# Performance work log

Hardware: AMD Instinct MI355X
Metric: run time of the kernel (lower is better)

The kernel has to match this reference:

```python
import jax, jax.numpy as jnp
import numpy as np

B, T, C, U, W = 8, 2048, 512, 512, 2


def setup_inputs() -> dict:
    key = jax.random.key(0)
    k1, k2 = jax.random.split(key)
    x = jax.random.normal(k1, (B, T, C), dtype=jnp.float32)
    # Conv1D kernel: [window, in_channels, 3*units] (z, f, o gates), glorot-ish scale
    kernel = jax.random.normal(k2, (W, C, 3 * U), dtype=jnp.float32) * (1.0 / np.sqrt(W * C))
    bias = jnp.zeros((3 * U,), dtype=jnp.float32)
    initial_state = jnp.zeros((1, U), dtype=jnp.float32)
    return {"x": x, "kernel": kernel, "bias": bias, "initial_state": initial_state}


def reference(x, kernel, bias, initial_state):
    # Causal Conv1D: pad (window-1) on the left of the time axis.
    window = kernel.shape[0]
    gates = jax.lax.conv_general_dilated(
        x, kernel,
        window_strides=(1,),
        padding=[(window - 1, 0)],
        dimension_numbers=("NWC", "WIO", "NWC"),
    ) + bias  # [B, T, 3U]
    z, f, o = jnp.split(gates, 3, axis=-1)
    z = jnp.tanh(z)
    f = jax.nn.sigmoid(f)
    o = jax.nn.sigmoid(o)

    # fo-pool recurrence: h_t = f_t * h_{t-1} + (1 - f_t) * z_t
    h0 = jnp.repeat(initial_state, x.shape[0], axis=0)  # [B, U]
    fs = jnp.moveaxis(f, 1, 0)  # [T, B, U]
    zs = jnp.moveaxis(z, 1, 0)  # [T, B, U]

    def step(h, fz):
        f_t, z_t = fz
        h = f_t * h + (1.0 - f_t) * z_t
        return h, h

    _, hs = jax.lax.scan(step, h0, (fs, zs))  # hs: [T, B, U]
    recurrent = jnp.moveaxis(hs, 0, 1)  # [B, T, U]

    # output gate, return_sequences=True
    return recurrent * o
```

## Files before the change

kernel.cpp:

```cpp
#include <hip/hip_runtime.h>


#define Bn 8
#define Tn 2048
#define Cn 512
#define Un 512
#define Nn 1536
#define Kn 1024
#define Mn (Bn * Tn)
#define NC 32
#define CL 64

using bf16x8 = __attribute__((ext_vector_type(8))) __bf16;
using f32x4  = __attribute__((ext_vector_type(4))) float;
using us8    = __attribute__((ext_vector_type(8))) unsigned short;

__device__ __forceinline__ void async16(const void* g, void* l) {
  __builtin_amdgcn_global_load_lds((const __attribute__((address_space(1))) void*)g,
                                   (__attribute__((address_space(3))) void*)l, 16, 0, 0);
}

__device__ __forceinline__ unsigned short f2bf(float v) {
  union { float f; unsigned u; } c; c.f = v;
  unsigned u = c.u;
  return (unsigned short)((u + 0x7fffu + ((u >> 16) & 1u)) >> 16);
}
__device__ __forceinline__ float asf(unsigned u) {
  union { unsigned u; float f; } c; c.u = u; return c.f;
}
__device__ __forceinline__ float bf_lo(unsigned w) { return asf(w << 16); }
__device__ __forceinline__ float bf_hi(unsigned w) { return asf(w & 0xffff0000u); }

__device__ __forceinline__ float fast_sigmoid(float x) {
  float e = __builtin_amdgcn_exp2f(-1.4426950408889634f * x);
  return __builtin_amdgcn_rcpf(1.0f + e);
}
__device__ __forceinline__ float fast_tanh(float x) {
  float e = __builtin_amdgcn_exp2f(-2.8853900817779268f * x);
  return 2.0f * __builtin_amdgcn_rcpf(1.0f + e) - 1.0f;
}

__global__ __launch_bounds__(256) void conv_x(const float* __restrict__ x,
                                              unsigned short* __restrict__ xb) {
  int idx = blockIdx.x * 256 + threadIdx.x;
  int c8  = idx & 63;
  int row = idx >> 6;
  int b   = row / (Tn + 1);
  int t   = row - b * (Tn + 1);
  us8 ov;
  if (t == 0) {
    ov = (us8)0;
  } else {
    const float* src = x + (size_t)(b * Tn + t - 1) * Cn + c8 * 8;
    float4 v0 = *(const float4*)src;
    float4 v1 = *(const float4*)(src + 4);
    ov[0] = f2bf(v0.x); ov[1] = f2bf(v0.y); ov[2] = f2bf(v0.z); ov[3] = f2bf(v0.w);
    ov[4] = f2bf(v1.x); ov[5] = f2bf(v1.y); ov[6] = f2bf(v1.z); ov[7] = f2bf(v1.w);
  }
  *(us8*)(xb + (size_t)row * Cn + c8 * 8) = ov;
}

__global__ __launch_bounds__(256) void conv_k(const float* __restrict__ kern,
                                              unsigned short* __restrict__ kT) {
  __shared__ float tile[32][33];
  int kb = blockIdx.x, nb = blockIdx.y;
  int tx = threadIdx.x & 31, ty = threadIdx.x >> 5;
#pragma unroll
  for (int i = 0; i < 4; i++)
    tile[ty + i * 8][tx] = kern[(size_t)(kb * 32 + ty + i * 8) * Nn + nb * 32 + tx];
  __syncthreads();
#pragma unroll
  for (int i = 0; i < 4; i++) {
    int n = nb * 32 + ty + i * 8;
    int k = kb * 32 + tx;
    kT[(size_t)n * Kn + k] = f2bf(tile[tx][ty + i * 8]);
  }
}

__global__ __launch_bounds__(256) void gemm_gates(const unsigned short* __restrict__ xb,
                                                  const unsigned short* __restrict__ kT,
                                                  const float* __restrict__ bias,
                                                  unsigned short* __restrict__ gates) {
  __shared__ unsigned short As[128 * 64];
  __shared__ unsigned short Bs[128 * 64];
  const int tid = threadIdx.x;
  const int m0 = blockIdx.x * 128;
  const int n0 = blockIdx.y * 128;
  const int batch = m0 / Tn;
  const int lane = tid & 63;
  const int w = tid >> 6, wr = w >> 1, wc = w & 1;

  const int srow = (w << 3) + (lane >> 3);
  const int skq  = (lane & 7) ^ (lane >> 3);
  const unsigned short* aStage = xb + (size_t)(m0 + batch + srow) * Cn + (skq << 3);
  const unsigned short* bStage = kT + (size_t)(n0 + srow) * Kn + (skq << 3);

  f32x4 zero = {0.f, 0.f, 0.f, 0.f};
  f32x4 acc[4][4];
#pragma unroll
  for (int i = 0; i < 4; i++)
#pragma unroll
    for (int j = 0; j < 4; j++) acc[i][j] = zero;

  const int rA0 = wr * 64 + (lane & 15);
  const int rB0 = wc * 64 + (lane & 15);
  const int swz = lane & 7;

  for (int k0 = 0; k0 < Kn; k0 += 64) {
#pragma unroll
    for (int j = 0; j < 4; j++) {
      async16(aStage + (size_t)(j << 5) * Cn + k0, &As[(j * 256 + tid) * 8]);
      async16(bStage + (size_t)(j << 5) * Kn + k0, &Bs[(j * 256 + tid) * 8]);
    }
    __builtin_amdgcn_s_waitcnt(0);
    __syncthreads();

#pragma unroll
    for (int ks = 0; ks < 2; ks++) {
      const int col = (((ks << 2) + (lane >> 4)) ^ swz) << 3;
      bf16x8 af[4], bf[4];
#pragma unroll
      for (int i = 0; i < 4; i++) {
        af[i] = *(const bf16x8*)&As[(rA0 + i * 16) * 64 + col];
        bf[i] = *(const bf16x8*)&Bs[(rB0 + i * 16) * 64 + col];
      }
#pragma unroll
      for (int i = 0; i < 4; i++)
#pragma unroll
        for (int j = 0; j < 4; j++)
          acc[i][j] = __builtin_amdgcn_mfma_f32_16x16x32_bf16(af[i], bf[j], acc[i][j], 0, 0, 0);
    }
    __syncthreads();
  }

  const int region = blockIdx.y >> 2;
  const int rowB = wr * 64 + (lane >> 4) * 4;
  const int colB = wc * 64 + (lane & 15);
#pragma unroll
  for (int i = 0; i < 4; i++)
#pragma unroll
    for (int j = 0; j < 4; j++)
#pragma unroll
      for (int r = 0; r < 4; r++) {
        int mm = m0 + rowB + i * 16 + r;
        int nn = n0 + colB + j * 16;
        float g = acc[i][j][r] + bias[nn];
        float a = (region == 0) ? fast_tanh(g) : fast_sigmoid(g);
        gates[(size_t)mm * Nn + nn] = f2bf(a);
      }
}

__global__ __launch_bounds__(256) void scan_phaseA(const unsigned short* __restrict__ gates,
                                                   unsigned int* __restrict__ ab) {
  int chunk = blockIdx.x;
  int b = chunk >> 5, c = chunk & (NC - 1);
  int u2 = threadIdx.x * 2;
  const unsigned short* gp = gates + (size_t)(b * Tn + c * CL) * Nn;
  float a0 = 1.f, a1 = 1.f, bv0 = 0.f, bv1 = 0.f;
#pragma unroll 8
  for (int t = 0; t < CL; t++) {
    unsigned zz = *(const unsigned*)(gp + u2);
    unsigned ff = *(const unsigned*)(gp + Un + u2);
    float z0 = bf_lo(zz), z1 = bf_hi(zz);
    float f0 = bf_lo(ff), f1 = bf_hi(ff);
    a0 *= f0; a1 *= f1;
    bv0 = f0 * bv0 + (1.0f - f0) * z0;
    bv1 = f1 * bv1 + (1.0f - f1) * z1;
    gp += Nn;
  }
  uint2 w;
  w.x = ((unsigned)f2bf(a0) << 16) | f2bf(bv0);
  w.y = ((unsigned)f2bf(a1) << 16) | f2bf(bv1);
  *(uint2*)(ab + (size_t)chunk * Un + u2) = w;
}

__global__ __launch_bounds__(256) void scan_phaseC(const unsigned short* __restrict__ gates,
                                                   const unsigned int* __restrict__ ab,
                                                   const float* __restrict__ init,
                                                   float* __restrict__ out) {
  int chunk = blockIdx.x;
  int b = chunk >> 5, c = chunk & (NC - 1);
  int u2 = threadIdx.x * 2;
  float h0 = init[u2], h1 = init[u2 + 1];
  for (int cp = 0; cp < c; cp++) {
    uint2 w = *(const uint2*)(ab + (size_t)(b * NC + cp) * Un + u2);
    h0 = asf(w.x & 0xffff0000u) * h0 + bf_lo(w.x);
    h1 = asf(w.y & 0xffff0000u) * h1 + bf_lo(w.y);
  }
  const unsigned short* gp = gates + (size_t)(b * Tn + c * CL) * Nn;
  float* op = out + (size_t)(b * Tn + c * CL) * Un;
#pragma unroll 8
  for (int t = 0; t < CL; t++) {
    unsigned zz = *(const unsigned*)(gp + u2);
    unsigned ff = *(const unsigned*)(gp + Un + u2);
    unsigned oo = *(const unsigned*)(gp + 2 * Un + u2);
    float z0 = bf_lo(zz), z1 = bf_hi(zz);
    float f0 = bf_lo(ff), f1 = bf_hi(ff);
    float o0 = bf_lo(oo), o1 = bf_hi(oo);
    h0 = f0 * h0 + (1.0f - f0) * z0;
    h1 = f1 * h1 + (1.0f - f1) * z1;
    float2 ov; ov.x = h0 * o0; ov.y = h1 * o1;
    *(float2*)(op + u2) = ov;
    gp += Nn;
    op += Un;
  }
}

extern "C" void kernel_launch(void* const* d_in, const int* in_sizes, int n_in,
                              void* d_out, int out_size, void* d_ws, size_t ws_size,
                              hipStream_t stream) {
  const float* x    = (const float*)d_in[0];
  const float* kern = (const float*)d_in[1];
  const float* bias = (const float*)d_in[2];
  const float* init = (const float*)d_in[3];
  float* out = (float*)d_out;

  char* ws = (char*)d_ws;
  unsigned short* xb = (unsigned short*)ws;
  size_t off = (size_t)Bn * (Tn + 1) * Cn * 2;
  unsigned short* kT = (unsigned short*)(ws + off);
  off += (size_t)Nn * Kn * 2;
  unsigned short* gates = (unsigned short*)(ws + off);
  off += (size_t)Mn * Nn * 2;
  unsigned int* ab = (unsigned int*)(ws + off);

  conv_x<<<(Bn * (Tn + 1) * Cn / 8) / 256, 256, 0, stream>>>(x, xb);
  conv_k<<<dim3(32, 48), 256, 0, stream>>>(kern, kT);
  gemm_gates<<<dim3(Mn / 128, Nn / 128), 256, 0, stream>>>(xb, kT, bias, gates);
  scan_phaseA<<<Bn * NC, 256, 0, stream>>>(gates, ab);
  scan_phaseC<<<Bn * NC, 256, 0, stream>>>(gates, ab, init, out);
}
```

Baseline: 178.1 us.

## Merge prep kernels, swap GEMM grid order, move activations into scan, widen scan grid

Merges the x and kernel conversion kernels into a single prep launch to drop one launch. Swaps the GEMM grid axes so that the blocks sharing one M tile of x are scheduled together, which improves L2 reuse of the A tile. Activations move out of the GEMM epilogue into the scan kernels, so the GEMM stores raw pre-activations and the scans recompute tanh/sigmoid, with phase A computing them a second time. Phase C now uses two blocks per chunk with one unit per thread, doubling parallelism but using narrower 2-byte loads.

```diff
diff --git a/kernel.cpp b/kernel.cpp
--- a/kernel.cpp
+++ b/kernel.cpp
@@ -28,6 +28,7 @@
 __device__ __forceinline__ float asf(unsigned u) {
   union { unsigned u; float f; } c; c.u = u; return c.f;
 }
+__device__ __forceinline__ float bf2f(unsigned short h) { return asf(((unsigned)h) << 16); }
 __device__ __forceinline__ float bf_lo(unsigned w) { return asf(w << 16); }
 __device__ __forceinline__ float bf_hi(unsigned w) { return asf(w & 0xffff0000u); }
 
@@ -40,40 +41,42 @@
   return 2.0f * __builtin_amdgcn_rcpf(1.0f + e) - 1.0f;
 }
 
-__global__ __launch_bounds__(256) void conv_x(const float* __restrict__ x,
-                                              unsigned short* __restrict__ xb) {
-  int idx = blockIdx.x * 256 + threadIdx.x;
-  int c8  = idx & 63;
-  int row = idx >> 6;
-  int b   = row / (Tn + 1);
-  int t   = row - b * (Tn + 1);
-  us8 ov;
-  if (t == 0) {
-    ov = (us8)0;
+__global__ __launch_bounds__(256) void prep(const float* __restrict__ x,
+                                            const float* __restrict__ kern,
+                                            unsigned short* __restrict__ xb,
+                                            unsigned short* __restrict__ kT) {
+  __shared__ float tile[32][33];
+  const int tid = threadIdx.x;
+  if (blockIdx.x < 1536) {
+    int kb = blockIdx.x & 31, nb = blockIdx.x >> 5;
+    int tx = tid & 31, ty = tid >> 5;
+#pragma unroll
+    for (int i = 0; i < 4; i++)
+      tile[ty + i * 8][tx] = kern[(size_t)(kb * 32 + ty + i * 8) * Nn + nb * 32 + tx];
+    __syncthreads();
+#pragma unroll
+    for (int i = 0; i < 4; i++) {
+      int n = nb * 32 + ty + i * 8;
+      int k = kb * 32 + tx;
+      kT[(size_t)n * Kn + k] = f2bf(tile[tx][ty + i * 8]);
+    }
   } else {
-    const float* src = x + (size_t)(b * Tn + t - 1) * Cn + c8 * 8;
-    float4 v0 = *(const float4*)src;
-    float4 v1 = *(const float4*)(src + 4);
-    ov[0] = f2bf(v0.x); ov[1] = f2bf(v0.y); ov[2] = f2bf(v0.z); ov[3] = f2bf(v0.w);
-    ov[4] = f2bf(v1.x); ov[5] = f2bf(v1.y); ov[6] = f2bf(v1.z); ov[7] = f2bf(v1.w);
-  }
-  *(us8*)(xb + (size_t)row * Cn + c8 * 8) = ov;
-}
-
-__global__ __launch_bounds__(256) void conv_k(const float* __restrict__ kern,
-                                              unsigned short* __restrict__ kT) {
-  __shared__ float tile[32][33];
-  int kb = blockIdx.x, nb = blockIdx.y;
-  int tx = threadIdx.x & 31, ty = threadIdx.x >> 5;
-#pragma unroll
-  for (int i = 0; i < 4; i++)
-    tile[ty + i * 8][tx] = kern[(size_t)(kb * 32 + ty + i * 8) * Nn + nb * 32 + tx];
-  __syncthreads();
-#pragma unroll
-  for (int i = 0; i < 4; i++) {
-    int n = nb * 32 + ty + i * 8;
-    int k = kb * 32 + tx;
-    kT[(size_t)n * Kn + k] = f2bf(tile[tx][ty + i * 8]);
+    int idx = (blockIdx.x - 1536) * 256 + tid;
+    int c8  = idx & 63;
+    int row = idx >> 6;
+    int b   = row / (Tn + 1);
+    int t   = row - b * (Tn + 1);
+    us8 ov;
+    if (t == 0) {
+      ov = (us8)0;
+    } else {
+      const float* src = x + (size_t)(b * Tn + t - 1) * Cn + c8 * 8;
+      float4 v0 = *(const float4*)src;
+      float4 v1 = *(const float4*)(src + 4);
+      ov[0] = f2bf(v0.x); ov[1] = f2bf(v0.y); ov[2] = f2bf(v0.z); ov[3] = f2bf(v0.w);
+      ov[4] = f2bf(v1.x); ov[5] = f2bf(v1.y); ov[6] = f2bf(v1.z); ov[7] = f2bf(v1.w);
+    }
+    *(us8*)(xb + (size_t)row * Cn + c8 * 8) = ov;
   }
 }
 
@@ -84,9 +87,9 @@
   __shared__ unsigned short As[128 * 64];
   __shared__ unsigned short Bs[128 * 64];
   const int tid = threadIdx.x;
-  const int m0 = blockIdx.x * 128;
-  const int n0 = blockIdx.y * 128;
-  const int batch = m0 / Tn;
+  const int m0 = blockIdx.y * 128;
+  const int n0 = blockIdx.x * 128;
+  const int batch = blockIdx.y >> 4;
   const int lane = tid & 63;
   const int w = tid >> 6, wr = w >> 1, wc = w & 1;
 
@@ -133,7 +136,6 @@
     __syncthreads();
   }
 
-  const int region = blockIdx.y >> 2;
   const int rowB = wr * 64 + (lane >> 4) * 4;
   const int colB = wc * 64 + (lane & 15);
 #pragma unroll
@@ -144,9 +146,7 @@
       for (int r = 0; r < 4; r++) {
         int mm = m0 + rowB + i * 16 + r;
         int nn = n0 + colB + j * 16;
-        float g = acc[i][j][r] + bias[nn];
-        float a = (region == 0) ? fast_tanh(g) : fast_sigmoid(g);
-        gates[(size_t)mm * Nn + nn] = f2bf(a);
+        gates[(size_t)mm * Nn + nn] = f2bf(acc[i][j][r] + bias[nn]);
       }
 }
 
@@ -161,8 +161,8 @@
   for (int t = 0; t < CL; t++) {
     unsigned zz = *(const unsigned*)(gp + u2);
     unsigned ff = *(const unsigned*)(gp + Un + u2);
-    float z0 = bf_lo(zz), z1 = bf_hi(zz);
-    float f0 = bf_lo(ff), f1 = bf_hi(ff);
+    float z0 = fast_tanh(bf_lo(zz)), z1 = fast_tanh(bf_hi(zz));
+    float f0 = fast_sigmoid(bf_lo(ff)), f1 = fast_sigmoid(bf_hi(ff));
     a0 *= f0; a1 *= f1;
     bv0 = f0 * bv0 + (1.0f - f0) * z0;
     bv1 = f1 * bv1 + (1.0f - f1) * z1;
@@ -178,29 +178,23 @@
                                                    const unsigned int* __restrict__ ab,
                                                    const float* __restrict__ init,
                                                    float* __restrict__ out) {
-  int chunk = blockIdx.x;
+  int chunk = blockIdx.x >> 1;
+  int u = (blockIdx.x & 1) * 256 + threadIdx.x;
   int b = chunk >> 5, c = chunk & (NC - 1);
-  int u2 = threadIdx.x * 2;
-  float h0 = init[u2], h1 = init[u2 + 1];
+  float h = init[u];
   for (int cp = 0; cp < c; cp++) {
-    uint2 w = *(const uint2*)(ab + (size_t)(b * NC + cp) * Un + u2);
-    h0 = asf(w.x & 0xffff0000u) * h0 + bf_lo(w.x);
-    h1 = asf(w.y & 0xffff0000u) * h1 + bf_lo(w.y);
+    unsigned wv = ab[(size_t)(b * NC + cp) * Un + u];
+    h = asf(wv & 0xffff0000u) * h + bf_lo(wv);
   }
   const unsigned short* gp = gates + (size_t)(b * Tn + c * CL) * Nn;
   float* op = out + (size_t)(b * Tn + c * CL) * Un;
 #pragma unroll 8
   for (int t = 0; t < CL; t++) {
-    unsigned zz = *(const unsigned*)(gp + u2);
-    unsigned ff = *(const unsigned*)(gp + Un + u2);
-    unsigned oo = *(const unsigned*)(gp + 2 * Un + u2);
-    float z0 = bf_lo(zz), z1 = bf_hi(zz);
-    float f0 = bf_lo(ff), f1 = bf_hi(ff);
-    float o0 = bf_lo(oo), o1 = bf_hi(oo);
-    h0 = f0 * h0 + (1.0f - f0) * z0;
-    h1 = f1 * h1 + (1.0f - f1) * z1;
-    float2 ov; ov.x = h0 * o0; ov.y = h1 * o1;
-    *(float2*)(op + u2) = ov;
+    float z = fast_tanh(bf2f(gp[u]));
+    float f = fast_sigmoid(bf2f(gp[Un + u]));
+    float o = fast_sigmoid(bf2f(gp[2 * Un + u]));
+    h = f * h + (1.0f - f) * z;
+    op[u] = h * o;
     gp += Nn;
     op += Un;
   }
@@ -224,9 +218,8 @@
   off += (size_t)Mn * Nn * 2;
   unsigned int* ab = (unsigned int*)(ws + off);
 
-  conv_x<<<(Bn * (Tn + 1) * Cn / 8) / 256, 256, 0, stream>>>(x, xb);
-  conv_k<<<dim3(32, 48), 256, 0, stream>>>(kern, kT);
-  gemm_gates<<<dim3(Mn / 128, Nn / 128), 256, 0, stream>>>(xb, kT, bias, gates);
+  prep<<<1536 + (Bn * (Tn + 1) * Cn / 8) / 256, 256, 0, stream>>>(x, kern, xb, kT);
+  gemm_gates<<<dim3(Nn / 128, Mn / 128), 256, 0, stream>>>(xb, kT, bias, gates);
   scan_phaseA<<<Bn * NC, 256, 0, stream>>>(gates, ab);
-  scan_phaseC<<<Bn * NC, 256, 0, stream>>>(gates, ab, init, out);
-}
+  scan_phaseC<<<Bn * NC * 2, 256, 0, stream>>>(gates, ab, init, out);
+}
```

Result: slower. 184.3 us (+3.5%).
